# Performance work log

Hardware: AMD Instinct MI355X
Metric: run time of the kernel (lower is better)

## Reference

```python
import jax, jax.numpy as jnp
import numpy as np

B, C, H, W = 8, 512, 48, 48
DK = C // 8            # query/key dim
L = max(H, W)          # rel_pos_length == H == W
R = 2 * L - 1          # num relative shifts
N = H * W
EPS = 1e-5


def setup_inputs() -> dict:
    key = jax.random.key(0)
    ks = jax.random.split(key, 20)
    d = {
        "x": jax.random.normal(ks[0], (B, C, H, W), jnp.float32),
        "Wq": jax.random.normal(ks[1], (DK, C), jnp.float32) * 0.02,
        "bq": jnp.zeros((DK,), jnp.float32),
        "q_scale": jnp.ones((DK,), jnp.float32),
        "q_bias": jnp.zeros((DK,), jnp.float32),
        "Wk": jax.random.normal(ks[2], (DK, C), jnp.float32) * 0.02,
        "bk": jnp.zeros((DK,), jnp.float32),
        "k_scale": jnp.ones((DK,), jnp.float32),
        "k_bias": jnp.zeros((DK,), jnp.float32),
        "Wv": jax.random.normal(ks[3], (C, C), jnp.float32) * 0.02,
        "bv": jnp.zeros((C,), jnp.float32),
        "v_scale": jnp.ones((C,), jnp.float32),
        "v_bias": jnp.zeros((C,), jnp.float32),
        "rel_rows": jax.random.normal(ks[4], (R, DK), jnp.float32),
        "rel_columns": jax.random.normal(ks[5], (R, DK), jnp.float32),
        "bnr_scale": jnp.ones((C,), jnp.float32),
        "bnr_bias": jnp.zeros((C,), jnp.float32),
        "bnc_scale": jnp.ones((C,), jnp.float32),
        "bnc_bias": jnp.zeros((C,), jnp.float32),
        # gamma is a learned scalar (init 0 in torch; nonzero here so output != x)
        "gamma": jax.random.normal(ks[6], (1,), jnp.float32) * 0.1,
    }
    return d


def _bn(y, scale, bias):
    # train-mode BatchNorm2d: batch stats over (B,H,W), biased variance
    m = jnp.mean(y, axis=(0, 2, 3))
    v = jnp.mean((y - m[None, :, None, None]) ** 2, axis=(0, 2, 3))
    yn = (y - m[None, :, None, None]) * jax.lax.rsqrt(v + EPS)[None, :, None, None]
    return yn * scale[None, :, None, None] + bias[None, :, None, None]


def _conv_bn_relu(x, Wc, bc, scale, bias):
    y = jnp.einsum('bchw,oc->bohw', x, Wc) + bc[None, :, None, None]  # 1x1 conv
    return jax.nn.relu(_bn(y, scale, bias))


def _rel_P(l, rel_table):
    # compute_reindexing_tensor reduces to a one-hot over shift (i - x) since
    # |i-x| <= L always holds when L == l; Ih @ rel_table == gather by shift.
    x = jnp.arange(l)[:, None]
    i = jnp.arange(l)[None, :]
    idx = i - x + (L - 1)                 # (l, l) in [0, 2L-2]
    return rel_table[idx]                 # (l, l, DK)


def reference(x, Wq, bq, q_scale, q_bias, Wk, bk, k_scale, k_bias,
              Wv, bv, v_scale, v_bias, rel_rows, rel_columns,
              bnr_scale, bnr_bias, bnc_scale, bnc_bias, gamma):
    q = _conv_bn_relu(x, Wq, bq, q_scale, q_bias).reshape(B, DK, N)   # proj_query^T
    k = _conv_bn_relu(x, Wk, bk, k_scale, k_bias).reshape(B, DK, N)
    v = _conv_bn_relu(x, Wv, bv, v_scale, v_bias).reshape(B, C, N)

    energy = jnp.einsum('bdn,bdm->bnm', q, k)        # (B,N,N) = Q^T K (unscaled)
    attention = jax.nn.softmax(energy, axis=-1)
    out = jnp.einsum('bcj,bij->bci', v, attention)   # V A^T
    attn_mask = out.reshape(B, C, H, W)

    # relative position terms: Eh = V (Ph Q^T), Ew = V (Pw Q^T)
    Ph = _rel_P(H, rel_rows).reshape(N, DK)          # (N,DK) since H==W
    Mh = jnp.einsum('nd,bdm->bnm', Ph, q)
    Eh = jnp.einsum('bcn,bnm->bcm', v, Mh).reshape(B, C, H, W)
    Eh = _bn(Eh, bnr_scale, bnr_bias)

    Pw = _rel_P(W, rel_columns).reshape(N, DK)
    Mw = jnp.einsum('nd,bdm->bnm', Pw, q)
    Ew = jnp.einsum('bcn,bnm->bcm', v, Mw).reshape(B, C, H, W)
    Ew = _bn(Ew, bnc_scale, bnc_bias)

    attn_mask = attn_mask + Eh + Ew
    return gamma[0] * attn_mask + x
```

## Files before the change

kernel.cpp:

```cpp
#include <hip/hip_runtime.h>
#include <math.h>

#define BB   8
#define CIN  512
#define NSP  2304
#define OCH  640
#define LL   48

#define AS1 __attribute__((address_space(1)))
#define AS3 __attribute__((address_space(3)))

typedef __attribute__((ext_vector_type(8))) short bf16x8;
typedef __attribute__((ext_vector_type(8))) unsigned short u16x8;
typedef __attribute__((ext_vector_type(4))) float f32x4;

__device__ inline unsigned short f2bf(float f) {
  unsigned int u = __float_as_uint(f);
  unsigned int r = (u + 0x7fffu + ((u >> 16) & 1u)) >> 16;
  return (unsigned short)r;
}
__device__ inline float bf2f(unsigned short h) {
  return __uint_as_float(((unsigned int)h) << 16);
}


#define STAGE128x64(GP, LD, LDSN)                                              \
  {                                                                            \
    const unsigned short* gsrc_ = (GP);                                        \
    _Pragma("unroll") for (int cc_ = 0; cc_ < 4; cc_++) {                      \
      int base_ = w * 2048 + cc_ * 512;                                        \
      int row_ = w * 32 + cc_ * 8 + rsub;                                      \
      __builtin_amdgcn_global_load_lds(                                        \
          (const AS1 void*)(gsrc_ + (size_t)row_ * (LD) + scolb),              \
          (AS3 void*)&(LDSN)[base_], 16, 0, 0);                                \
    }                                                                          \
  }

#define STAGE8(GPA, LDA, LA, GPB, LDB, LB)                                     \
  {                                                                            \
    if (w < 4) {                                                               \
      const unsigned short* gsrc_ = (GPA);                                     \
      _Pragma("unroll") for (int cc_ = 0; cc_ < 4; cc_++) {                    \
        int base_ = w * 2048 + cc_ * 512;                                      \
        int row_ = w * 32 + cc_ * 8 + rsub;                                    \
        __builtin_amdgcn_global_load_lds(                                      \
            (const AS1 void*)(gsrc_ + (size_t)row_ * (LDA) + scolb),           \
            (AS3 void*)&(LA)[base_], 16, 0, 0);                                \
      }                                                                        \
    } else {                                                                   \
      const unsigned short* gsrc_ = (GPB);                                     \
      int w2_ = w - 4;                                                         \
      _Pragma("unroll") for (int cc_ = 0; cc_ < 4; cc_++) {                    \
        int base_ = w2_ * 2048 + cc_ * 512;                                    \
        int row_ = w2_ * 32 + cc_ * 8 + rsub;                                  \
        __builtin_amdgcn_global_load_lds(                                      \
            (const AS1 void*)(gsrc_ + (size_t)row_ * (LDB) + scolb),           \
            (AS3 void*)&(LB)[base_], 16, 0, 0);                                \
      }                                                                        \
    }                                                                          \
  }

#define MFMA_STEP(APTR, BPTR)                                                  \
  _Pragma("unroll") for (int kk_ = 0; kk_ < 2; kk_++) {                        \
    bf16x8 af_[4], bf_[4];                                                     \
    int kcol_ = (((kk_ * 4 + (lane >> 4)) ^ (lane & 7)) * 8);                  \
    _Pragma("unroll") for (int m_ = 0; m_ < 4; m_++)                           \
      af_[m_] = *(const bf16x8*)&(APTR)[(wr * 64 + m_ * 16 + (lane & 15)) * 64 + kcol_]; \
    _Pragma("unroll") for (int n_ = 0; n_ < 4; n_++)                           \
      bf_[n_] = *(const bf16x8*)&(BPTR)[(wc * 64 + n_ * 16 + (lane & 15)) * 64 + kcol_]; \
    _Pragma("unroll") for (int m_ = 0; m_ < 4; m_++)                           \
      _Pragma("unroll") for (int n_ = 0; n_ < 4; n_++)                         \
        acc[m_][n_] = __builtin_amdgcn_mfma_f32_16x16x32_bf16(                 \
            af_[m_], bf_[n_], acc[m_][n_], 0, 0, 0);                           \
  }

#define MFMA_STEP8(APTR, BPTR)                                                 \
  _Pragma("unroll") for (int kk_ = 0; kk_ < 2; kk_++) {                        \
    bf16x8 af_[4], bf_[2];                                                     \
    int kcol_ = (((kk_ * 4 + (lane >> 4)) ^ (lane & 7)) * 8);                  \
    _Pragma("unroll") for (int m_ = 0; m_ < 4; m_++)                           \
      af_[m_] = *(const bf16x8*)&(APTR)[(wr * 64 + m_ * 16 + (lane & 15)) * 64 + kcol_]; \
    _Pragma("unroll") for (int n_ = 0; n_ < 2; n_++)                           \
      bf_[n_] = *(const bf16x8*)&(BPTR)[(wc * 32 + n_ * 16 + (lane & 15)) * 64 + kcol_]; \
    _Pragma("unroll") for (int m_ = 0; m_ < 4; m_++)                           \
      _Pragma("unroll") for (int n_ = 0; n_ < 2; n_++)                         \
        acc[m_][n_] = __builtin_amdgcn_mfma_f32_16x16x32_bf16(                 \
            af_[m_], bf_[n_], acc[m_][n_], 0, 0, 0);                           \
  }

#define MFMA_PROLOG()                                                          \
  const int tid = threadIdx.x;                                                 \
  const int lane = tid & 63;                                                   \
  const int w = tid >> 6;                                                      \
  const int wr = w >> 1, wc = w & 1;                                           \
  const int rsub = lane >> 3;                                                  \
  const int scolb = ((lane & 7) ^ rsub) * 8;                                   \
  f32x4 acc[4][4] = {};                                                        \
  (void)scolb; (void)rsub; (void)wr; (void)wc;

__global__ __launch_bounds__(256) void prep_all(
    const float* __restrict__ Wq, const float* __restrict__ bq,
    const float* __restrict__ Wk, const float* __restrict__ bk,
    const float* __restrict__ Wv, const float* __restrict__ bv,
    const float* __restrict__ rel_rows, const float* __restrict__ rel_cols,
    unsigned short* __restrict__ Wstb, float* __restrict__ bst,
    unsigned short* __restrict__ Pcatb) {
  int idx = blockIdx.x * 256 + threadIdx.x;
  if (idx < OCH * CIN) {
    int row = idx >> 9;
    float val;
    if (row < 64)       val = Wq[idx];
    else if (row < 128) val = Wk[idx - (64 << 9)];
    else                val = Wv[idx - (128 << 9)];
    Wstb[idx] = f2bf(val);
    if (idx < OCH) {
      float bval;
      if (idx < 64)       bval = bq[idx];
      else if (idx < 128) bval = bk[idx - 64];
      else                bval = bv[idx - 128];
      bst[idx] = bval;
    }
  } else {
    int p = idx - OCH * CIN;
    int dd = p / NSP;
    int n = p - dd * NSP;
    int xr = n / LL;
    int ic = n - xr * LL;
    int shift = ic - xr + (LL - 1);
    float val = (dd < 64) ? rel_rows[shift * 64 + dd]
                          : rel_cols[shift * 64 + (dd - 64)];
    Pcatb[p] = f2bf(val);
  }
}

__global__ __launch_bounds__(256) void transpose_x(
    const float* __restrict__ x, unsigned short* __restrict__ xTb) {
  __shared__ float t[64][65];
  const int n0 = blockIdx.x * 64;
  const int c0 = blockIdx.y * 64;
  const int b = blockIdx.z;
  const int j = threadIdx.x & 63;
  const int g = threadIdx.x >> 6;
  const float* xp = x + (size_t)b * CIN * NSP;
#pragma unroll
  for (int i = 0; i < 16; i++) {
    int cl = g * 16 + i;
    t[cl][j] = xp[(size_t)(c0 + cl) * NSP + n0 + j];
  }
  __syncthreads();
  unsigned short* op = xTb + (size_t)b * NSP * CIN;
#pragma unroll
  for (int i = 0; i < 16; i++) {
    int nl = g * 16 + i;
    op[(size_t)(n0 + nl) * CIN + c0 + j] = f2bf(t[j][nl]);
  }
}

__global__ __launch_bounds__(256) void proj_mfma(
    const unsigned short* __restrict__ Wstb, const float* __restrict__ bst,
    const unsigned short* __restrict__ xTb, unsigned short* __restrict__ y16,
    float* __restrict__ part1, float* __restrict__ part2) {
  __shared__ unsigned short As[2][8192];
  __shared__ unsigned short Bs[2][8192];
  int sw = ((blockIdx.x & 7) * 90) + (blockIdx.x >> 3);
  const int rb = sw % 5;
  const int nb = (sw / 5) % 18;
  const int b = sw / 90;
  const int r0 = rb * 128;
// ... 116 lines not shown
    ushort4 o0, o1;
    o0.x = f2bf(fmaxf(0.f, a * bf2f(u0.x) + bo));
    o0.y = f2bf(fmaxf(0.f, a * bf2f(u0.y) + bo));
    o0.z = f2bf(fmaxf(0.f, a * bf2f(u0.z) + bo));
    o0.w = f2bf(fmaxf(0.f, a * bf2f(u0.w) + bo));
    o1.x = f2bf(fmaxf(0.f, a * bf2f(u1.x) + bo));
    o1.y = f2bf(fmaxf(0.f, a * bf2f(u1.y) + bo));
    o1.z = f2bf(fmaxf(0.f, a * bf2f(u1.z) + bo));
    o1.w = f2bf(fmaxf(0.f, a * bf2f(u1.w) + bo));
    *(ushort4*)&y16[off] = o0;
    *(ushort4*)&y16[off + 4] = o1;
    if (ch < 128) {
      *(ushort4*)&qk[ch][n8] = o0;
      *(ushort4*)&qk[ch][n8 + 4] = o1;
    }
  }
  __syncthreads();
#pragma unroll
  for (int it = 0; it < 4; it++) {
    int combo = (tid >> 6) + it * 4;
    int plane = combo >> 3;
    int dg = combo & 7;
    int nl = tid & 63;
    unsigned short tmp[8];
#pragma unroll
    for (int d = 0; d < 8; d++) tmp[d] = qk[plane * 64 + dg * 8 + d][nl];
    unsigned short* out = (plane == 0) ? qTb : kTb;
    *(u16x8*)&out[((size_t)b * NSP + n0 + nl) * 64 + dg * 8] = *(u16x8*)tmp;
  }
}

__global__ __launch_bounds__(256) void gq_mfma(
    const unsigned short* __restrict__ y16, float* __restrict__ Gqp,
    float* __restrict__ qsp) {
  __shared__ float wlds[4 * 4096];
  const int bx = blockIdx.x;
  const int b = bx >> 2, kc = bx & 3;
  const int tid = threadIdx.x;
  const int lane = tid & 63;
  const int w = tid >> 6;
  const unsigned short* q = y16 + (size_t)b * OCH * NSP;
  f32x4 acc[4][4] = {};
  for (int k0 = kc * 576 + w * 32; k0 < (kc + 1) * 576; k0 += 128) {
    bf16x8 fr[4];
#pragma unroll
    for (int f = 0; f < 4; f++) {
      int row = f * 16 + (lane & 15);
      fr[f] = *(const bf16x8*)&q[(size_t)row * NSP + k0 + (lane >> 4) * 8];
    }
#pragma unroll
    for (int fm = 0; fm < 4; fm++)
#pragma unroll
      for (int fn = 0; fn < 4; fn++)
        acc[fm][fn] = __builtin_amdgcn_mfma_f32_16x16x32_bf16(
            fr[fm], fr[fn], acc[fm][fn], 0, 0, 0);
  }
#pragma unroll
  for (int fm = 0; fm < 4; fm++)
#pragma unroll
    for (int fn = 0; fn < 4; fn++)
#pragma unroll
      for (int r = 0; r < 4; r++) {
        int d = fm * 16 + (lane >> 4) * 4 + r;
        int e = fn * 16 + (lane & 15);
        wlds[w * 4096 + d * 64 + e] = acc[fm][fn][r];
      }
  {
    float s = 0.f;
    const unsigned short* qrow = q + (size_t)(tid >> 2) * NSP + kc * 576 + (tid & 3) * 144;
    for (int i = 0; i < 144; i += 4) {
      ushort4 u = *(const ushort4*)&qrow[i];
      s += bf2f(u.x) + bf2f(u.y) + bf2f(u.z) + bf2f(u.w);
    }
    s += __shfl_down(s, 1);
    s += __shfl_down(s, 2);
    if ((tid & 3) == 0) qsp[bx * 64 + (tid >> 2)] = s;
  }
  __syncthreads();
  for (int t = tid; t < 4096; t += 256)
    Gqp[(size_t)bx * 4096 + t] =
        wlds[t] + wlds[4096 + t] + wlds[8192 + t] + wlds[12288 + t];
}

__global__ __launch_bounds__(256) void energy_mfma(
    const unsigned short* __restrict__ qTb, const unsigned short* __restrict__ kTb,
    unsigned short* __restrict__ Pp, float* __restrict__ Ppart) {
  __shared__ unsigned short lds[16384];
  __shared__ float rs[256];
  int sw = ((blockIdx.x & 7) * 324) + (blockIdx.x >> 3);
  const int jb = sw % 18;
  const int ib = (sw / 18) % 18;
  const int b = sw / 324;
  const int i0 = ib * 128;
  const int j0 = jb * 128;
  MFMA_PROLOG();
  STAGE128x64(qTb + ((size_t)b * NSP + i0) * 64, 64, lds);
  STAGE128x64(kTb + ((size_t)b * NSP + j0) * 64, 64, (lds + 8192));
  __syncthreads();
  MFMA_STEP(lds, (lds + 8192));
  __syncthreads();
#pragma unroll
  for (int m = 0; m < 4; m++) {
#pragma unroll
    for (int r = 0; r < 4; r++) {
      int rl = wr * 64 + m * 16 + (lane >> 4) * 4 + r;
      float s1 = 0.f;
#pragma unroll
      for (int n = 0; n < 4; n++) {
        unsigned short h = f2bf(__expf(acc[m][n][r]));
        lds[rl * 128 + wc * 64 + n * 16 + (lane & 15)] = h;
        s1 += bf2f(h);
      }
#pragma unroll
      for (int off = 1; off < 16; off <<= 1) s1 += __shfl_xor(s1, off);
      if ((lane & 15) == 0) rs[rl * 2 + wc] = s1;
    }
  }
  __syncthreads();
  unsigned short* pp = Pp + (size_t)b * NSP * NSP;
#pragma unroll
  for (int c8 = tid; c8 < 2048; c8 += 256) {
    int il = c8 >> 4;
    int jl = (c8 & 15) * 8;
    u16x8 v = *(const u16x8*)&lds[il * 128 + jl];
    *(u16x8*)&pp[(size_t)(i0 + il) * NSP + j0 + jl] = v;
  }
  if (tid < 128)
    Ppart[((size_t)b * 18 + jb) * NSP + i0 + tid] = rs[tid * 2] + rs[tid * 2 + 1];
}

__global__ __launch_bounds__(256) void up_mfma(
    const unsigned short* __restrict__ y16, const unsigned short* __restrict__ Pcatb,
    float* __restrict__ Upart) {
  __shared__ unsigned short As[2][8192];
  __shared__ unsigned short Bs[2][8192];
  int sw = ((blockIdx.x & 7) * 24) + (blockIdx.x >> 3);
  const int cb = sw % 4;
  const int kc = (sw / 4) % 6;
  const int b = sw / 24;
  const int c0 = cb * 128;
  MFMA_PROLOG();
  const unsigned short* A = y16 + ((size_t)b * OCH + 128 + c0) * NSP + kc * 384;
  const unsigned short* B = Pcatb + kc * 384;

  STAGE128x64(A, NSP, As[0]);
  STAGE128x64(B, NSP, Bs[0]);
  asm volatile("s_waitcnt vmcnt(0)" ::: "memory");
  __builtin_amdgcn_sched_barrier(0);
  __builtin_amdgcn_s_barrier();

  int cur = 0;
  for (int t = 0; t < 6; ++t) {
    if (t + 1 < 6) {
      STAGE128x64(A + (t + 1) * 64, NSP, As[cur ^ 1]);
      STAGE128x64(B + (t + 1) * 64, NSP, Bs[cur ^ 1]);
    }
    __builtin_amdgcn_s_setprio(1);
    MFMA_STEP(As[cur], Bs[cur]);
    __builtin_amdgcn_s_setprio(0);
    asm volatile("s_waitcnt vmcnt(0)" ::: "memory");
    __builtin_amdgcn_sched_barrier(0);
    __builtin_amdgcn_s_barrier();
    cur ^= 1;
  }

  float* up = Upart + ((size_t)kc * BB + b) * CIN * 128 + (size_t)c0 * 128;
#pragma unroll
  for (int m = 0; m < 4; m++)
#pragma unroll
    for (int r = 0; r < 4; r++) {
      int rl = wr * 64 + m * 16 + (lane >> 4) * 4 + r;
#pragma unroll
      for (int n = 0; n < 4; n++) {
        int col = wc * 64 + n * 16 + (lane & 15);
        up[(size_t)rl * 128 + col] = acc[m][n][r];
      }
    }
}

__global__ __launch_bounds__(256) void rel_finalize(
    const float* __restrict__ Upart, const float* __restrict__ Gqp,
    const float* __restrict__ qsp,
    const float* __restrict__ bnr_s, const float* __restrict__ bnr_b,
    const float* __restrict__ bnc_s, const float* __restrict__ bnc_b,
    float* __restrict__ offc, unsigned short* __restrict__ Ucb) {
  const int c = blockIdx.x;
  const int tid = threadIdx.x;
  __shared__ float U[8][128];
  __shared__ float ghw[2];
  for (int t = tid; t < 1024; t += 256) {
    int b = t >> 7, dd = t & 127;
    float s = 0.f;
#pragma unroll
    for (int kc = 0; kc < 6; kc++)
      s += Upart[(((size_t)kc * BB + b) * CIN + c) * 128 + dd];
    U[b][dd] = s;
  }
  __syncthreads();
  if (tid < 64) {
    const int d = tid;
    float s1h = 0.f, s2h = 0.f, s1w = 0.f, s2w = 0.f;
    for (int b = 0; b < BB; b++) {
      float uh = U[b][d], uw = U[b][64 + d];
      float th = 0.f, tw = 0.f;
      float qsd = 0.f;
#pragma unroll
      for (int kc = 0; kc < 4; kc++) {
        const float* G = Gqp + ((size_t)(b * 4 + kc)) * 4096 + d * 64;
        for (int e = 0; e < 64; e++) {
          float g = G[e];
          th += g * U[b][e];
          tw += g * U[b][64 + e];
        }
        qsd += qsp[(b * 4 + kc) * 64 + d];
      }
      s1h += uh * qsd;
      s2h += uh * th;
      s1w += uw * qsd;
      s2w += uw * tw;
    }
#pragma unroll
    for (int off = 32; off > 0; off >>= 1) {
      s1h += __shfl_down(s1h, off);
      s2h += __shfl_down(s2h, off);
      s1w += __shfl_down(s1w, off);
      s2w += __shfl_down(s2w, off);
    }
    if (d == 0) {
      const float inv = 1.f / (float)(BB * NSP);
      float mh = s1h * inv, vh = s2h * inv - mh * mh;
      float mw = s1w * inv, vw = s2w * inv - mw * mw;
      float gch = bnr_s[c] * rsqrtf(vh + 1e-5f);
      float gcw = bnc_s[c] * rsqrtf(vw + 1e-5f);
      ghw[0] = gch;
      ghw[1] = gcw;
      offc[c] = (bnr_b[c] - mh * gch) + (bnc_b[c] - mw * gcw);
    }
  }
  __syncthreads();
  for (int t = tid; t < 512; t += 256) {
    int b = t >> 6, d = t & 63;
    Ucb[((size_t)b * CIN + c) * 64 + d] =
        f2bf(U[b][d] * ghw[0] + U[b][64 + d] * ghw[1]);
  }
}

__global__ __launch_bounds__(512) void attn_fused_gemm(
    const unsigned short* __restrict__ y16,
    const unsigned short* __restrict__ Pp,
    const float* __restrict__ Ppart,
    const unsigned short* __restrict__ Ucb,
    const unsigned short* __restrict__ qTb,
    const float* __restrict__ offc,
    const float* __restrict__ gammap,
    const float* __restrict__ x,
    float* __restrict__ dst) {
  __shared__ unsigned short As[4][8192];
  __shared__ unsigned short Bs[4][8192];
  __shared__ float rzl[128];
  int sw = ((blockIdx.x & 7) * 72) + (blockIdx.x >> 3);
  const int cb = sw % 4;
  const int ib = (sw / 4) % 18;
  const int b = sw / 72;
  const int c0 = cb * 128;
  const int i0 = ib * 128;
  const int tid = threadIdx.x;
  const int lane = tid & 63;
  const int w = tid >> 6;
  const int wr = w >> 2, wc = w & 3;
  const int rsub = lane >> 3;
  const int scolb = ((lane & 7) ^ rsub) * 8;
  const int l15 = lane & 15, l4 = lane >> 4;
  f32x4 acc[4][2] = {};

  const unsigned short* A = y16 + ((size_t)b * OCH + 128 + c0) * NSP;
  const unsigned short* B = Pp + (size_t)b * NSP * NSP + (size_t)i0 * NSP;
  const unsigned short* A2 = Ucb + (size_t)b * CIN * 64 + (size_t)c0 * 64;
  const unsigned short* B2 = qTb + ((size_t)b * NSP + i0) * 64;

  if (tid < 128) {
    float s = 0.f;
#pragma unroll
    for (int jb = 0; jb < 18; jb++)
      s += Ppart[((size_t)b * 18 + jb) * NSP + i0 + tid];
    rzl[tid] = 1.f / s;
  }
  asm volatile("s_waitcnt lgkmcnt(0)" ::: "memory");
  __builtin_amdgcn_sched_barrier(0);

  STAGE8(A, NSP, As[0], B, NSP, Bs[0]);
  STAGE8(A + 64, NSP, As[1], B + 64, NSP, Bs[1]);

  for (int t = 0; t < 37; ++t) {
    if (t + 2 < 36) {
      STAGE8(A + (t + 2) * 64, NSP, As[(t + 2) & 3], B + (t + 2) * 64, NSP, Bs[(t + 2) & 3]);
      asm volatile("s_waitcnt vmcnt(8)" ::: "memory");
    } else if (t + 2 == 36) {
      STAGE8(A2, 64, As[(t + 2) & 3], B2, 64, Bs[(t + 2) & 3]);
      asm volatile("s_waitcnt vmcnt(8)" ::: "memory");
    } else if (t + 1 <= 36) {
      asm volatile("s_waitcnt vmcnt(4)" ::: "memory");
    } else {
      asm volatile("s_waitcnt vmcnt(0)" ::: "memory");
    }
    __builtin_amdgcn_sched_barrier(0);
    __builtin_amdgcn_s_barrier();
    if (t == 36) {
#pragma unroll
      for (int n = 0; n < 2; n++) {
        float rz = rzl[wc * 32 + n * 16 + l15];
#pragma unroll
        for (int m = 0; m < 4; m++)
#pragma unroll
          for (int r = 0; r < 4; r++) acc[m][n][r] *= rz;
      }
    }
    __builtin_amdgcn_s_setprio(1);
    MFMA_STEP8(As[t & 3], Bs[t & 3]);
    __builtin_amdgcn_s_setprio(0);
  }

  const float gmm = gammap[0];
  const float* xp = x + (size_t)b * CIN * NSP;
  float* dp = dst + (size_t)b * CIN * NSP;
#pragma unroll
  for (int m = 0; m < 4; m++) {
#pragma unroll
    for (int r = 0; r < 4; r++) {
      int c = c0 + wr * 64 + m * 16 + l4 * 4 + r;
      float off = offc[c];
#pragma unroll
      for (int n = 0; n < 2; n++) {
        int i = i0 + wc * 32 + n * 16 + l15;
        size_t o = (size_t)c * NSP + i;
        dp[o] = gmm * (acc[m][n][r] + off) + xp[o];
      }
    }
  }
}

extern "C" void kernel_launch(void* const* d_in, const int* in_sizes, int n_in,
                              void* d_out, int out_size, void* d_ws, size_t ws_size,
                              hipStream_t stream) {
  const float* x        = (const float*)d_in[0];
  const float* Wq       = (const float*)d_in[1];
  const float* bq       = (const float*)d_in[2];
  const float* q_scale  = (const float*)d_in[3];
  const float* q_bias   = (const float*)d_in[4];
  const float* Wk       = (const float*)d_in[5];
  const float* bk       = (const float*)d_in[6];
  const float* k_scale  = (const float*)d_in[7];
  const float* k_bias   = (const float*)d_in[8];
  const float* Wv       = (const float*)d_in[9];
  const float* bv       = (const float*)d_in[10];
  const float* v_scale  = (const float*)d_in[11];
  const float* v_bias   = (const float*)d_in[12];
  const float* rel_rows = (const float*)d_in[13];
  const float* rel_cols = (const float*)d_in[14];
  const float* bnr_s    = (const float*)d_in[15];
  const float* bnr_b    = (const float*)d_in[16];
  const float* bnc_s    = (const float*)d_in[17];
  const float* bnc_b    = (const float*)d_in[18];
  const float* gamma    = (const float*)d_in[19];
  float* dst = (float*)d_out;

  float* ws = (float*)d_ws;
  size_t o = 0;
  unsigned short* Wstb = (unsigned short*)(ws + o); o += (size_t)OCH * CIN / 2;
  float* bst    = ws + o; o += 1024;
  float* chanA  = ws + o; o += 1024;
  float* chanB  = ws + o; o += 1024;
  unsigned short* Pcatb = (unsigned short*)(ws + o); o += (size_t)128 * NSP / 2;
  unsigned short* y16 = (unsigned short*)(ws + o); o += (size_t)BB * OCH * NSP / 2;
  unsigned short* xTb = (unsigned short*)(ws + o); o += (size_t)BB * NSP * CIN / 2;
  unsigned short* Pp  = (unsigned short*)(ws + o); o += (size_t)BB * NSP * NSP / 2;
  float* Ppart  = ws + o; o += (size_t)BB * 18 * NSP;
  float* Upart  = ws + o; o += (size_t)6 * BB * CIN * 128;
  float* Gqp    = ws + o; o += (size_t)32 * 4096;
  float* part1  = ws + o; o += (size_t)BB * 18 * OCH;
  float* part2  = ws + o; o += (size_t)BB * 18 * OCH;
  float* qsp    = ws + o; o += (size_t)32 * 64;
  float* offc   = ws + o; o += 1024;
  unsigned short* qTb = (unsigned short*)(ws + o); o += (size_t)BB * NSP * 64 / 2;
  unsigned short* kTb = (unsigned short*)(ws + o); o += (size_t)BB * NSP * 64 / 2;
  unsigned short* Ucb = (unsigned short*)(ws + o); o += (size_t)BB * CIN * 64 / 2;

  prep_all<<<(OCH * CIN + 128 * NSP) / 256, 256, 0, stream>>>(
      Wq, bq, Wk, bk, Wv, bv, rel_rows, rel_cols, Wstb, bst, Pcatb);
  transpose_x<<<dim3(NSP / 64, CIN / 64, BB), 256, 0, stream>>>(x, xTb);

  proj_mfma<<<720, 256, 0, stream>>>(Wstb, bst, xTb, y16, part1, part2);
  bn_finalize<<<OCH, 256, 0, stream>>>(part1, part2, q_scale, q_bias, k_scale,
                                       k_bias, v_scale, v_bias, chanA, chanB);
  bn_post<<<dim3(36, BB), 256, 0, stream>>>(y16, chanA, chanB, qTb, kTb);
  gq_mfma<<<32, 256, 0, stream>>>(y16, Gqp, qsp);

  energy_mfma<<<2592, 256, 0, stream>>>(qTb, kTb, Pp, Ppart);

  up_mfma<<<192, 256, 0, stream>>>(y16, Pcatb, Upart);
  rel_finalize<<<CIN, 256, 0, stream>>>(Upart, Gqp, qsp, bnr_s, bnr_b,
                                        bnc_s, bnc_b, offc, Ucb);

  attn_fused_gemm<<<576, 512, 0, stream>>>(y16, Pp, Ppart, Ucb, qTb, offc,
                                           gamma, x, dst);
}
```

Baseline: 245.0 us.

## Fuse energy/softmax computation into attention GEMM flash-style, drop materialized P

Removes the separate energy kernel that wrote the full B×N×N bf16 exp(QK^T) matrix plus row partial sums to global memory. The attention kernel now recomputes each 128×64 energy tile from q/k staged in LDS, exponentiates it into an LDS P tile, and accumulates row sums in registers for the final normalization. This avoids roughly 85 MB of global writes and reads. In exchange, exp and QK^T are recomputed once per channel block (4x redundancy), and there are extra barriers per step with only single-buffered V/P.

```diff
diff --git a/kernel.cpp b/kernel.cpp
--- a/kernel.cpp
+++ b/kernel.cpp
@@ -33,30 +33,6 @@
       __builtin_amdgcn_global_load_lds(                                        \
           (const AS1 void*)(gsrc_ + (size_t)row_ * (LD) + scolb),              \
           (AS3 void*)&(LDSN)[base_], 16, 0, 0);                                \
-    }                                                                          \
-  }
-
-#define STAGE8(GPA, LDA, LA, GPB, LDB, LB)                                     \
-  {                                                                            \
-    if (w < 4) {                                                               \
-      const unsigned short* gsrc_ = (GPA);                                     \
-      _Pragma("unroll") for (int cc_ = 0; cc_ < 4; cc_++) {                    \
-        int base_ = w * 2048 + cc_ * 512;                                      \
-        int row_ = w * 32 + cc_ * 8 + rsub;                                    \
-        __builtin_amdgcn_global_load_lds(                                      \
-            (const AS1 void*)(gsrc_ + (size_t)row_ * (LDA) + scolb),           \
-            (AS3 void*)&(LA)[base_], 16, 0, 0);                                \
-      }                                                                        \
-    } else {                                                                   \
-      const unsigned short* gsrc_ = (GPB);                                     \
-      int w2_ = w - 4;                                                         \
-      _Pragma("unroll") for (int cc_ = 0; cc_ < 4; cc_++) {                    \
-        int base_ = w2_ * 2048 + cc_ * 512;                                    \
-        int row_ = w2_ * 32 + cc_ * 8 + rsub;                                  \
-        __builtin_amdgcn_global_load_lds(                                      \
-            (const AS1 void*)(gsrc_ + (size_t)row_ * (LDB) + scolb),           \
-            (AS3 void*)&(LB)[base_], 16, 0, 0);                                \
-      }                                                                        \
     }                                                                          \
   }
 
@@ -366,53 +342,6 @@
         wlds[t] + wlds[4096 + t] + wlds[8192 + t] + wlds[12288 + t];
 }
 
-__global__ __launch_bounds__(256) void energy_mfma(
-    const unsigned short* __restrict__ qTb, const unsigned short* __restrict__ kTb,
-    unsigned short* __restrict__ Pp, float* __restrict__ Ppart) {
-  __shared__ unsigned short lds[16384];
-  __shared__ float rs[256];
-  int sw = ((blockIdx.x & 7) * 324) + (blockIdx.x >> 3);
-  const int jb = sw % 18;
-  const int ib = (sw / 18) % 18;
-  const int b = sw / 324;
-  const int i0 = ib * 128;
-  const int j0 = jb * 128;
-  MFMA_PROLOG();
-  STAGE128x64(qTb + ((size_t)b * NSP + i0) * 64, 64, lds);
-  STAGE128x64(kTb + ((size_t)b * NSP + j0) * 64, 64, (lds + 8192));
-  __syncthreads();
-  MFMA_STEP(lds, (lds + 8192));
-  __syncthreads();
-#pragma unroll
-  for (int m = 0; m < 4; m++) {
-#pragma unroll
-    for (int r = 0; r < 4; r++) {
-      int rl = wr * 64 + m * 16 + (lane >> 4) * 4 + r;
-      float s1 = 0.f;
-#pragma unroll
-      for (int n = 0; n < 4; n++) {
-        unsigned short h = f2bf(__expf(acc[m][n][r]));
-        lds[rl * 128 + wc * 64 + n * 16 + (lane & 15)] = h;
-        s1 += bf2f(h);
-      }
-#pragma unroll
-      for (int off = 1; off < 16; off <<= 1) s1 += __shfl_xor(s1, off);
-      if ((lane & 15) == 0) rs[rl * 2 + wc] = s1;
-    }
-  }
-  __syncthreads();
-  unsigned short* pp = Pp + (size_t)b * NSP * NSP;
-#pragma unroll
-  for (int c8 = tid; c8 < 2048; c8 += 256) {
-    int il = c8 >> 4;
-    int jl = (c8 & 15) * 8;
-    u16x8 v = *(const u16x8*)&lds[il * 128 + jl];
-    *(u16x8*)&pp[(size_t)(i0 + il) * NSP + j0 + jl] = v;
-  }
-  if (tid < 128)
-    Ppart[((size_t)b * 18 + jb) * NSP + i0 + tid] = rs[tid * 2] + rs[tid * 2 + 1];
-}
-
 __global__ __launch_bounds__(256) void up_mfma(
     const unsigned short* __restrict__ y16, const unsigned short* __restrict__ Pcatb,
     float* __restrict__ Upart) {
@@ -529,18 +458,20 @@
   }
 }
 
-__global__ __launch_bounds__(512) void attn_fused_gemm(
+__global__ __launch_bounds__(512) void attn_flash2(
     const unsigned short* __restrict__ y16,
-    const unsigned short* __restrict__ Pp,
-    const float* __restrict__ Ppart,
+    const unsigned short* __restrict__ qTb,
+    const unsigned short* __restrict__ kTb,
     const unsigned short* __restrict__ Ucb,
-    const unsigned short* __restrict__ qTb,
     const float* __restrict__ offc,
     const float* __restrict__ gammap,
     const float* __restrict__ x,
     float* __restrict__ dst) {
-  __shared__ unsigned short As[4][8192];
-  __shared__ unsigned short Bs[4][8192];
+  __shared__ unsigned short q_lds[8192];
+  __shared__ unsigned short k_lds[2][4096];
+  __shared__ unsigned short v_lds[8192];
+  __shared__ unsigned short p_lds[8192];
+  __shared__ float rsum_lds[8][64];
   __shared__ float rzl[128];
   int sw = ((blockIdx.x & 7) * 72) + (blockIdx.x >> 3);
   const int cb = sw % 4;
@@ -552,57 +483,136 @@
   const int lane = tid & 63;
   const int w = tid >> 6;
   const int wr = w >> 2, wc = w & 3;
+  const int iSub = w >> 2, jSub = w & 3;
   const int rsub = lane >> 3;
   const int scolb = ((lane & 7) ^ rsub) * 8;
   const int l15 = lane & 15, l4 = lane >> 4;
   f32x4 acc[4][2] = {};
-
-  const unsigned short* A = y16 + ((size_t)b * OCH + 128 + c0) * NSP;
-  const unsigned short* B = Pp + (size_t)b * NSP * NSP + (size_t)i0 * NSP;
-  const unsigned short* A2 = Ucb + (size_t)b * CIN * 64 + (size_t)c0 * 64;
-  const unsigned short* B2 = qTb + ((size_t)b * NSP + i0) * 64;
-
-  if (tid < 128) {
-    float s = 0.f;
-#pragma unroll
-    for (int jb = 0; jb < 18; jb++)
-      s += Ppart[((size_t)b * 18 + jb) * NSP + i0 + tid];
-    rzl[tid] = 1.f / s;
-  }
-  asm volatile("s_waitcnt lgkmcnt(0)" ::: "memory");
+  float rs[4][4] = {{0.f}};
+
+  const unsigned short* qsrc = qTb + ((size_t)b * NSP + i0) * 64;
+  const unsigned short* ksrc = kTb + (size_t)b * NSP * 64;
+  const unsigned short* vsrc = y16 + ((size_t)b * OCH + 128 + c0) * NSP;
+
+#pragma unroll
+  for (int i = 0; i < 2; i++) {
+    int row = w * 16 + i * 8 + rsub;
+    __builtin_amdgcn_global_load_lds(
+        (const AS1 void*)(qsrc + (size_t)row * 64 + scolb),
+        (AS3 void*)&q_lds[w * 1024 + i * 512], 16, 0, 0);
+  }
+  if (w >= 4) {
+    int w4 = w - 4;
+#pragma unroll
+    for (int i = 0; i < 2; i++) {
+      int row = w4 * 16 + i * 8 + rsub;
+      __builtin_amdgcn_global_load_lds(
+          (const AS1 void*)(ksrc + (size_t)row * 64 + scolb),
+          (AS3 void*)&k_lds[0][w4 * 1024 + i * 512], 16, 0, 0);
+    }
+  }
+  asm volatile("s_waitcnt vmcnt(0)" ::: "memory");
   __builtin_amdgcn_sched_barrier(0);
-
-  STAGE8(A, NSP, As[0], B, NSP, Bs[0]);
-  STAGE8(A + 64, NSP, As[1], B + 64, NSP, Bs[1]);
-
-  for (int t = 0; t < 37; ++t) {
-    if (t + 2 < 36) {
-      STAGE8(A + (t + 2) * 64, NSP, As[(t + 2) & 3], B + (t + 2) * 64, NSP, Bs[(t + 2) & 3]);
-      asm volatile("s_waitcnt vmcnt(8)" ::: "memory");
-    } else if (t + 2 == 36) {
-      STAGE8(A2, 64, As[(t + 2) & 3], B2, 64, Bs[(t + 2) & 3]);
-      asm volatile("s_waitcnt vmcnt(8)" ::: "memory");
-    } else if (t + 1 <= 36) {
-      asm volatile("s_waitcnt vmcnt(4)" ::: "memory");
-    } else {
-      asm volatile("s_waitcnt vmcnt(0)" ::: "memory");
-    }
+  __builtin_amdgcn_s_barrier();
+
+  for (int t = 0; t < 36; ++t) {
+    const int cur = t & 1;
+    if (w < 4) {
+#pragma unroll
+      for (int cc = 0; cc < 4; cc++) {
+        int row = w * 32 + cc * 8 + rsub;
+        __builtin_amdgcn_global_load_lds(
+            (const AS1 void*)(vsrc + (size_t)row * NSP + t * 64 + scolb),
+            (AS3 void*)&v_lds[w * 2048 + cc * 512], 16, 0, 0);
+      }
+    } else if (t + 1 < 36) {
+      int w4 = w - 4;
+#pragma unroll
+      for (int i = 0; i < 2; i++) {
+        int row = (t + 1) * 64 + w4 * 16 + i * 8 + rsub;
+        __builtin_amdgcn_global_load_lds(
+            (const AS1 void*)(ksrc + (size_t)row * 64 + scolb),
+            (AS3 void*)&k_lds[cur ^ 1][w4 * 1024 + i * 512], 16, 0, 0);
+      }
+    }
+    f32x4 eacc[4] = {};
+#pragma unroll
+    for (int kk = 0; kk < 2; kk++) {
+      int kcol = ((kk * 4 + l4) ^ (lane & 7)) * 8;
+      bf16x8 bk = *(const bf16x8*)&k_lds[cur][(jSub * 16 + l15) * 64 + kcol];
+#pragma unroll
+      for (int m = 0; m < 4; m++) {
+        bf16x8 aq = *(const bf16x8*)&q_lds[(iSub * 64 + m * 16 + l15) * 64 + kcol];
+        eacc[m] = __builtin_amdgcn_mfma_f32_16x16x32_bf16(aq, bk, eacc[m], 0, 0, 0);
+      }
+    }
+#pragma unroll
+    for (int m = 0; m < 4; m++) {
+#pragma unroll
+      for (int r = 0; r < 4; r++) {
+        float p = __expf(eacc[m][r]);
+        unsigned short h = f2bf(p);
+        rs[m][r] += bf2f(h);
+        int il = iSub * 64 + m * 16 + l4 * 4 + r;
+        int j = jSub * 16 + l15;
+        p_lds[il * 64 + ((j >> 3) ^ (il & 7)) * 8 + (j & 7)] = h;
+      }
+    }
+    asm volatile("s_waitcnt lgkmcnt(0)" ::: "memory");
+    if (w < 4) asm volatile("s_waitcnt vmcnt(0)" ::: "memory");
     __builtin_amdgcn_sched_barrier(0);
     __builtin_amdgcn_s_barrier();
-    if (t == 36) {
-#pragma unroll
-      for (int n = 0; n < 2; n++) {
-        float rz = rzl[wc * 32 + n * 16 + l15];
-#pragma unroll
-        for (int m = 0; m < 4; m++)
-#pragma unroll
-          for (int r = 0; r < 4; r++) acc[m][n][r] *= rz;
-      }
-    }
     __builtin_amdgcn_s_setprio(1);
-    MFMA_STEP8(As[t & 3], Bs[t & 3]);
+    MFMA_STEP8(v_lds, p_lds);
     __builtin_amdgcn_s_setprio(0);
-  }
+    if (w >= 4) asm volatile("s_waitcnt vmcnt(0)" ::: "memory");
+    __builtin_amdgcn_sched_barrier(0);
+    __builtin_amdgcn_s_barrier();
+  }
+
+  if (w < 4) {
+    const unsigned short* a2 = Ucb + (size_t)b * CIN * 64 + (size_t)c0 * 64;
+#pragma unroll
+    for (int cc = 0; cc < 4; cc++) {
+      int row = w * 32 + cc * 8 + rsub;
+      __builtin_amdgcn_global_load_lds(
+          (const AS1 void*)(a2 + (size_t)row * 64 + scolb),
+          (AS3 void*)&v_lds[w * 2048 + cc * 512], 16, 0, 0);
+    }
+  }
+#pragma unroll
+  for (int m = 0; m < 4; m++) {
+#pragma unroll
+    for (int r = 0; r < 4; r++) {
+      float s = rs[m][r];
+      s += __shfl_xor(s, 1);
+      s += __shfl_xor(s, 2);
+      s += __shfl_xor(s, 4);
+      s += __shfl_xor(s, 8);
+      if (l15 == 0) rsum_lds[w][m * 16 + l4 * 4 + r] = s;
+    }
+  }
+  asm volatile("s_waitcnt lgkmcnt(0)" ::: "memory");
+  if (w < 4) asm volatile("s_waitcnt vmcnt(0)" ::: "memory");
+  __builtin_amdgcn_sched_barrier(0);
+  __builtin_amdgcn_s_barrier();
+  if (tid < 128) {
+    int is = tid >> 6, il = tid & 63;
+    rzl[tid] = 1.f / (rsum_lds[is * 4 + 0][il] + rsum_lds[is * 4 + 1][il] +
+                      rsum_lds[is * 4 + 2][il] + rsum_lds[is * 4 + 3][il]);
+  }
+  __syncthreads();
+
+#pragma unroll
+  for (int n = 0; n < 2; n++) {
+    float rz = rzl[wc * 32 + n * 16 + l15];
+#pragma unroll
+    for (int m = 0; m < 4; m++)
+#pragma unroll
+      for (int r = 0; r < 4; r++) acc[m][n][r] *= rz;
+  }
+
+  MFMA_STEP8(v_lds, q_lds);
 
   const float gmm = gammap[0];
   const float* xp = x + (size_t)b * CIN * NSP;
@@ -657,8 +667,6 @@
   unsigned short* Pcatb = (unsigned short*)(ws + o); o += (size_t)128 * NSP / 2;
   unsigned short* y16 = (unsigned short*)(ws + o); o += (size_t)BB * OCH * NSP / 2;
   unsigned short* xTb = (unsigned short*)(ws + o); o += (size_t)BB * NSP * CIN / 2;
-  unsigned short* Pp  = (unsigned short*)(ws + o); o += (size_t)BB * NSP * NSP / 2;
-  float* Ppart  = ws + o; o += (size_t)BB * 18 * NSP;
   float* Upart  = ws + o; o += (size_t)6 * BB * CIN * 128;
   float* Gqp    = ws + o; o += (size_t)32 * 4096;
   float* part1  = ws + o; o += (size_t)BB * 18 * OCH;
@@ -679,12 +687,9 @@
   bn_post<<<dim3(36, BB), 256, 0, stream>>>(y16, chanA, chanB, qTb, kTb);
   gq_mfma<<<32, 256, 0, stream>>>(y16, Gqp, qsp);
 
-  energy_mfma<<<2592, 256, 0, stream>>>(qTb, kTb, Pp, Ppart);
-
   up_mfma<<<192, 256, 0, stream>>>(y16, Pcatb, Upart);
   rel_finalize<<<CIN, 256, 0, stream>>>(Upart, Gqp, qsp, bnr_s, bnr_b,
                                         bnc_s, bnc_b, offc, Ucb);
 
-  attn_fused_gemm<<<576, 512, 0, stream>>>(y16, Pp, Ppart, Ucb, qTb, offc,
-                                           gamma, x, dst);
-}
+  attn_flash2<<<576, 512, 0, stream>>>(y16, qTb, kTb, Ucb, offc, gamma, x, dst);
+}
```

Measured after the change: 302.4 us. 23.4% more time.

## Widen attn_fused_gemm tile to 128x256 with double-buffered LDS pipeline

Applied to the files above, without the earlier changes.

The final fused attention GEMM now computes a 128-channel by 256-position output tile per block instead of 128x128. This halves the grid to 288 blocks and doubles the per-wave accumulator tile to 4x4 MFMA fragments. The 4-stage, prefetch-distance-2 LDS ring is replaced by a simple double buffer that waits on all loads after each step. The larger tile is meant to cut repeated reads of the A operand (y16 V rows) and raise MFMA work per LDS load. The trade-off is higher register pressure, fewer blocks than CUs for occupancy, and a shallower prefetch that may expose memory latency.

```diff
diff --git a/kernel.cpp b/kernel.cpp
--- a/kernel.cpp
+++ b/kernel.cpp
@@ -36,30 +36,6 @@
     }                                                                          \
   }
 
-#define STAGE8(GPA, LDA, LA, GPB, LDB, LB)                                     \
-  {                                                                            \
-    if (w < 4) {                                                               \
-      const unsigned short* gsrc_ = (GPA);                                     \
-      _Pragma("unroll") for (int cc_ = 0; cc_ < 4; cc_++) {                    \
-        int base_ = w * 2048 + cc_ * 512;                                      \
-        int row_ = w * 32 + cc_ * 8 + rsub;                                    \
-        __builtin_amdgcn_global_load_lds(                                      \
-            (const AS1 void*)(gsrc_ + (size_t)row_ * (LDA) + scolb),           \
-            (AS3 void*)&(LA)[base_], 16, 0, 0);                                \
-      }                                                                        \
-    } else {                                                                   \
-      const unsigned short* gsrc_ = (GPB);                                     \
-      int w2_ = w - 4;                                                         \
-      _Pragma("unroll") for (int cc_ = 0; cc_ < 4; cc_++) {                    \
-        int base_ = w2_ * 2048 + cc_ * 512;                                    \
-        int row_ = w2_ * 32 + cc_ * 8 + rsub;                                  \
-        __builtin_amdgcn_global_load_lds(                                      \
-            (const AS1 void*)(gsrc_ + (size_t)row_ * (LDB) + scolb),           \
-            (AS3 void*)&(LB)[base_], 16, 0, 0);                                \
-      }                                                                        \
-    }                                                                          \
-  }
-
 #define MFMA_STEP(APTR, BPTR)                                                  \
   _Pragma("unroll") for (int kk_ = 0; kk_ < 2; kk_++) {                        \
     bf16x8 af_[4], bf_[4];                                                     \
@@ -70,20 +46,6 @@
       bf_[n_] = *(const bf16x8*)&(BPTR)[(wc * 64 + n_ * 16 + (lane & 15)) * 64 + kcol_]; \
     _Pragma("unroll") for (int m_ = 0; m_ < 4; m_++)                           \
       _Pragma("unroll") for (int n_ = 0; n_ < 4; n_++)                         \
-        acc[m_][n_] = __builtin_amdgcn_mfma_f32_16x16x32_bf16(                 \
-            af_[m_], bf_[n_], acc[m_][n_], 0, 0, 0);                           \
-  }
-
-#define MFMA_STEP8(APTR, BPTR)                                                 \
-  _Pragma("unroll") for (int kk_ = 0; kk_ < 2; kk_++) {                        \
-    bf16x8 af_[4], bf_[2];                                                     \
-    int kcol_ = (((kk_ * 4 + (lane >> 4)) ^ (lane & 7)) * 8);                  \
-    _Pragma("unroll") for (int m_ = 0; m_ < 4; m_++)                           \
-      af_[m_] = *(const bf16x8*)&(APTR)[(wr * 64 + m_ * 16 + (lane & 15)) * 64 + kcol_]; \
-    _Pragma("unroll") for (int n_ = 0; n_ < 2; n_++)                           \
-      bf_[n_] = *(const bf16x8*)&(BPTR)[(wc * 32 + n_ * 16 + (lane & 15)) * 64 + kcol_]; \
-    _Pragma("unroll") for (int m_ = 0; m_ < 4; m_++)                           \
-      _Pragma("unroll") for (int n_ = 0; n_ < 2; n_++)                         \
         acc[m_][n_] = __builtin_amdgcn_mfma_f32_16x16x32_bf16(                 \
             af_[m_], bf_[n_], acc[m_][n_], 0, 0, 0);                           \
   }
@@ -539,15 +501,15 @@
     const float* __restrict__ gammap,
     const float* __restrict__ x,
     float* __restrict__ dst) {
-  __shared__ unsigned short As[4][8192];
-  __shared__ unsigned short Bs[4][8192];
-  __shared__ float rzl[128];
-  int sw = ((blockIdx.x & 7) * 72) + (blockIdx.x >> 3);
+  __shared__ unsigned short As[2][8192];
+  __shared__ unsigned short Bs[2][16384];
+  __shared__ float rzl[256];
+  int sw = ((blockIdx.x & 7) * 36) + (blockIdx.x >> 3);
   const int cb = sw % 4;
-  const int ib = (sw / 4) % 18;
-  const int b = sw / 72;
+  const int ib = (sw / 4) % 9;
+  const int b = sw / 36;
   const int c0 = cb * 128;
-  const int i0 = ib * 128;
+  const int i0 = ib * 256;
   const int tid = threadIdx.x;
   const int lane = tid & 63;
   const int w = tid >> 6;
@@ -555,53 +517,71 @@
   const int rsub = lane >> 3;
   const int scolb = ((lane & 7) ^ rsub) * 8;
   const int l15 = lane & 15, l4 = lane >> 4;
-  f32x4 acc[4][2] = {};
+  f32x4 acc[4][4] = {};
 
   const unsigned short* A = y16 + ((size_t)b * OCH + 128 + c0) * NSP;
   const unsigned short* B = Pp + (size_t)b * NSP * NSP + (size_t)i0 * NSP;
   const unsigned short* A2 = Ucb + (size_t)b * CIN * 64 + (size_t)c0 * 64;
   const unsigned short* B2 = qTb + ((size_t)b * NSP + i0) * 64;
 
-  if (tid < 128) {
+#define STAGEF(GPA, LDA, LA, GPB, LDB, LB)                                     \
+  {                                                                            \
+    if (w < 4) {                                                               \
+      const unsigned short* ga_ = (GPA);                                       \
+      _Pragma("unroll") for (int cc_ = 0; cc_ < 4; cc_++) {                    \
+        int row_ = w * 32 + cc_ * 8 + rsub;                                    \
+        __builtin_amdgcn_global_load_lds(                                      \
+            (const AS1 void*)(ga_ + (size_t)row_ * (LDA) + scolb),             \
+            (AS3 void*)&(LA)[w * 2048 + cc_ * 512], 16, 0, 0);                 \
+      }                                                                        \
+    }                                                                          \
+    {                                                                          \
+      const unsigned short* gb_ = (GPB);                                       \
+      _Pragma("unroll") for (int cc_ = 0; cc_ < 4; cc_++) {                    \
+        int row_ = w * 32 + cc_ * 8 + rsub;                                    \
+        __builtin_amdgcn_global_load_lds(                                      \
+            (const AS1 void*)(gb_ + (size_t)row_ * (LDB) + scolb),             \
+            (AS3 void*)&(LB)[w * 2048 + cc_ * 512], 16, 0, 0);                 \
+      }                                                                        \
+    }                                                                          \
+  }
+
+  if (tid < 256) {
     float s = 0.f;
 #pragma unroll
     for (int jb = 0; jb < 18; jb++)
       s += Ppart[((size_t)b * 18 + jb) * NSP + i0 + tid];
     rzl[tid] = 1.f / s;
   }
-  asm volatile("s_waitcnt lgkmcnt(0)" ::: "memory");
+  STAGEF(A, NSP, As[0], B, NSP, Bs[0]);
+  asm volatile("s_waitcnt vmcnt(0)" ::: "memory");
   __builtin_amdgcn_sched_barrier(0);
-
-  STAGE8(A, NSP, As[0], B, NSP, Bs[0]);
-  STAGE8(A + 64, NSP, As[1], B + 64, NSP, Bs[1]);
-
+  __builtin_amdgcn_s_barrier();
+
+  int cur = 0;
   for (int t = 0; t < 37; ++t) {
-    if (t + 2 < 36) {
-      STAGE8(A + (t + 2) * 64, NSP, As[(t + 2) & 3], B + (t + 2) * 64, NSP, Bs[(t + 2) & 3]);
-      asm volatile("s_waitcnt vmcnt(8)" ::: "memory");
-    } else if (t + 2 == 36) {
-      STAGE8(A2, 64, As[(t + 2) & 3], B2, 64, Bs[(t + 2) & 3]);
-      asm volatile("s_waitcnt vmcnt(8)" ::: "memory");
-    } else if (t + 1 <= 36) {
-      asm volatile("s_waitcnt vmcnt(4)" ::: "memory");
-    } else {
-      asm volatile("s_waitcnt vmcnt(0)" ::: "memory");
-    }
+    if (t + 1 < 36) {
+      STAGEF(A + (t + 1) * 64, NSP, As[cur ^ 1], B + (t + 1) * 64, NSP, Bs[cur ^ 1]);
+    } else if (t + 1 == 36) {
+      STAGEF(A2, 64, As[cur ^ 1], B2, 64, Bs[cur ^ 1]);
+    }
+    if (t == 36) {
+#pragma unroll
+      for (int n = 0; n < 4; n++) {
+        float rz = rzl[wc * 64 + n * 16 + l15];
+#pragma unroll
+        for (int m = 0; m < 4; m++)
+#pragma unroll
+          for (int r = 0; r < 4; r++) acc[m][n][r] *= rz;
+      }
+    }
+    __builtin_amdgcn_s_setprio(1);
+    MFMA_STEP(As[cur], Bs[cur]);
+    __builtin_amdgcn_s_setprio(0);
+    asm volatile("s_waitcnt vmcnt(0)" ::: "memory");
     __builtin_amdgcn_sched_barrier(0);
     __builtin_amdgcn_s_barrier();
-    if (t == 36) {
-#pragma unroll
-      for (int n = 0; n < 2; n++) {
-        float rz = rzl[wc * 32 + n * 16 + l15];
-#pragma unroll
-        for (int m = 0; m < 4; m++)
-#pragma unroll
-          for (int r = 0; r < 4; r++) acc[m][n][r] *= rz;
-      }
-    }
-    __builtin_amdgcn_s_setprio(1);
-    MFMA_STEP8(As[t & 3], Bs[t & 3]);
-    __builtin_amdgcn_s_setprio(0);
+    cur ^= 1;
   }
 
   const float gmm = gammap[0];
@@ -614,13 +594,14 @@
       int c = c0 + wr * 64 + m * 16 + l4 * 4 + r;
       float off = offc[c];
 #pragma unroll
-      for (int n = 0; n < 2; n++) {
-        int i = i0 + wc * 32 + n * 16 + l15;
+      for (int n = 0; n < 4; n++) {
+        int i = i0 + wc * 64 + n * 16 + l15;
         size_t o = (size_t)c * NSP + i;
         dp[o] = gmm * (acc[m][n][r] + off) + xp[o];
       }
     }
   }
+#undef STAGEF
 }
 
 extern "C" void kernel_launch(void* const* d_in, const int* in_sizes, int n_in,
@@ -685,6 +666,6 @@
   rel_finalize<<<CIN, 256, 0, stream>>>(Upart, Gqp, qsp, bnr_s, bnr_b,
                                         bnc_s, bnc_b, offc, Ucb);
 
-  attn_fused_gemm<<<576, 512, 0, stream>>>(y16, Pp, Ppart, Ucb, qTb, offc,
+  attn_fused_gemm<<<288, 512, 0, stream>>>(y16, Pp, Ppart, Ucb, qTb, offc,
                                            gamma, x, dst);
 }
```

After: 267.0 us. 9.0% more time.

## Widen energy tiles to 128x256 with 512 threads; double-buffer fused attention GEMM

Applied to the files above, without the earlier changes.

The energy kernel now computes a 128x256 tile per 512-thread block, so each Q tile is loaded once and reused across two K tiles. Loads go directly to LDS, and the exp/bf16 write-out is done in two halves that reuse the K buffer. The fused attention GEMM drops from a 4-stage pipeline with a 2-ahead prefetch to a 2-stage double buffer that waits on vmcnt(0) every iteration. This halves that kernel's LDS use, which may raise occupancy, but it hides less memory latency.

```diff
diff --git a/kernel.cpp b/kernel.cpp
--- a/kernel.cpp
+++ b/kernel.cpp
@@ -366,51 +366,110 @@
         wlds[t] + wlds[4096 + t] + wlds[8192 + t] + wlds[12288 + t];
 }
 
-__global__ __launch_bounds__(256) void energy_mfma(
+__global__ __launch_bounds__(512) void energy_mfma(
     const unsigned short* __restrict__ qTb, const unsigned short* __restrict__ kTb,
     unsigned short* __restrict__ Pp, float* __restrict__ Ppart) {
-  __shared__ unsigned short lds[16384];
-  __shared__ float rs[256];
-  int sw = ((blockIdx.x & 7) * 324) + (blockIdx.x >> 3);
-  const int jb = sw % 18;
-  const int ib = (sw / 18) % 18;
-  const int b = sw / 324;
+  __shared__ unsigned short q_lds[8192];
+  __shared__ unsigned short k_lds[16384];
+  __shared__ float rs_lds[4][128];
+  int sw = ((blockIdx.x & 7) * 162) + (blockIdx.x >> 3);
+  const int jp = sw % 9;
+  const int ib = (sw / 9) % 18;
+  const int b = sw / 162;
   const int i0 = ib * 128;
-  const int j0 = jb * 128;
-  MFMA_PROLOG();
-  STAGE128x64(qTb + ((size_t)b * NSP + i0) * 64, 64, lds);
-  STAGE128x64(kTb + ((size_t)b * NSP + j0) * 64, 64, (lds + 8192));
-  __syncthreads();
-  MFMA_STEP(lds, (lds + 8192));
-  __syncthreads();
-#pragma unroll
-  for (int m = 0; m < 4; m++) {
-#pragma unroll
-    for (int r = 0; r < 4; r++) {
-      int rl = wr * 64 + m * 16 + (lane >> 4) * 4 + r;
-      float s1 = 0.f;
-#pragma unroll
-      for (int n = 0; n < 4; n++) {
-        unsigned short h = f2bf(__expf(acc[m][n][r]));
-        lds[rl * 128 + wc * 64 + n * 16 + (lane & 15)] = h;
-        s1 += bf2f(h);
-      }
-#pragma unroll
-      for (int off = 1; off < 16; off <<= 1) s1 += __shfl_xor(s1, off);
-      if ((lane & 15) == 0) rs[rl * 2 + wc] = s1;
-    }
-  }
-  __syncthreads();
+  const int j0 = jp * 256;
+  const int tid = threadIdx.x;
+  const int lane = tid & 63;
+  const int w = tid >> 6;
+  const int wr = w >> 2, wc = w & 3;
+  const int rsub = lane >> 3;
+  const int scolb = ((lane & 7) ^ rsub) * 8;
+  const int l15 = lane & 15, l4 = lane >> 4;
+  f32x4 acc[4][4] = {};
+
+  if (w < 4) {
+    const unsigned short* gq = qTb + ((size_t)b * NSP + i0) * 64;
+#pragma unroll
+    for (int cc = 0; cc < 4; cc++) {
+      int row = w * 32 + cc * 8 + rsub;
+      __builtin_amdgcn_global_load_lds(
+          (const AS1 void*)(gq + (size_t)row * 64 + scolb),
+          (AS3 void*)&q_lds[w * 2048 + cc * 512], 16, 0, 0);
+    }
+  }
+  {
+    const unsigned short* gk = kTb + ((size_t)b * NSP + j0) * 64;
+#pragma unroll
+    for (int cc = 0; cc < 4; cc++) {
+      int row = w * 32 + cc * 8 + rsub;
+      __builtin_amdgcn_global_load_lds(
+          (const AS1 void*)(gk + (size_t)row * 64 + scolb),
+          (AS3 void*)&k_lds[w * 2048 + cc * 512], 16, 0, 0);
+    }
+  }
+  asm volatile("s_waitcnt vmcnt(0)" ::: "memory");
+  __builtin_amdgcn_sched_barrier(0);
+  __builtin_amdgcn_s_barrier();
+
+#pragma unroll
+  for (int kk = 0; kk < 2; kk++) {
+    bf16x8 af[4], bf[4];
+    int kcol = ((kk * 4 + l4) ^ (lane & 7)) * 8;
+#pragma unroll
+    for (int m = 0; m < 4; m++)
+      af[m] = *(const bf16x8*)&q_lds[(wr * 64 + m * 16 + l15) * 64 + kcol];
+#pragma unroll
+    for (int n = 0; n < 4; n++)
+      bf[n] = *(const bf16x8*)&k_lds[(wc * 64 + n * 16 + l15) * 64 + kcol];
+#pragma unroll
+    for (int m = 0; m < 4; m++)
+#pragma unroll
+      for (int n = 0; n < 4; n++)
+        acc[m][n] = __builtin_amdgcn_mfma_f32_16x16x32_bf16(
+            af[m], bf[n], acc[m][n], 0, 0, 0);
+  }
+  __builtin_amdgcn_s_barrier();
+
   unsigned short* pp = Pp + (size_t)b * NSP * NSP;
 #pragma unroll
-  for (int c8 = tid; c8 < 2048; c8 += 256) {
-    int il = c8 >> 4;
-    int jl = (c8 & 15) * 8;
-    u16x8 v = *(const u16x8*)&lds[il * 128 + jl];
-    *(u16x8*)&pp[(size_t)(i0 + il) * NSP + j0 + jl] = v;
-  }
-  if (tid < 128)
-    Ppart[((size_t)b * 18 + jb) * NSP + i0 + tid] = rs[tid * 2] + rs[tid * 2 + 1];
+  for (int h = 0; h < 2; h++) {
+    if ((wc >> 1) == h) {
+#pragma unroll
+      for (int m = 0; m < 4; m++) {
+#pragma unroll
+        for (int r = 0; r < 4; r++) {
+          int rl = wr * 64 + m * 16 + l4 * 4 + r;
+          float s1 = 0.f;
+#pragma unroll
+          for (int n = 0; n < 4; n++) {
+            unsigned short hh = f2bf(__expf(acc[m][n][r]));
+            k_lds[rl * 128 + (wc & 1) * 64 + n * 16 + l15] = hh;
+            s1 += bf2f(hh);
+          }
+#pragma unroll
+          for (int off = 1; off < 16; off <<= 1) s1 += __shfl_xor(s1, off);
+          if (l15 == 0) rs_lds[wc][rl] = s1;
+        }
+      }
+    }
+    asm volatile("s_waitcnt lgkmcnt(0)" ::: "memory");
+    __builtin_amdgcn_sched_barrier(0);
+    __builtin_amdgcn_s_barrier();
+#pragma unroll
+    for (int it = 0; it < 4; it++) {
+      int c8 = tid + it * 512;
+      int il = c8 >> 4;
+      int jl = (c8 & 15) * 8;
+      u16x8 v = *(const u16x8*)&k_lds[il * 128 + jl];
+      *(u16x8*)&pp[(size_t)(i0 + il) * NSP + j0 + h * 128 + jl] = v;
+    }
+    __builtin_amdgcn_s_barrier();
+  }
+  if (tid < 256) {
+    int jbh = tid >> 7, i = tid & 127;
+    Ppart[((size_t)b * 18 + jp * 2 + jbh) * NSP + i0 + i] =
+        rs_lds[jbh * 2][i] + rs_lds[jbh * 2 + 1][i];
+  }
 }
 
 __global__ __launch_bounds__(256) void up_mfma(
@@ -539,8 +598,8 @@
     const float* __restrict__ gammap,
     const float* __restrict__ x,
     float* __restrict__ dst) {
-  __shared__ unsigned short As[4][8192];
-  __shared__ unsigned short Bs[4][8192];
+  __shared__ unsigned short As[2][8192];
+  __shared__ unsigned short Bs[2][8192];
   __shared__ float rzl[128];
   int sw = ((blockIdx.x & 7) * 72) + (blockIdx.x >> 3);
   const int cb = sw % 4;
@@ -573,35 +632,34 @@
   __builtin_amdgcn_sched_barrier(0);
 
   STAGE8(A, NSP, As[0], B, NSP, Bs[0]);
-  STAGE8(A + 64, NSP, As[1], B + 64, NSP, Bs[1]);
-
-  for (int t = 0; t < 37; ++t) {
-    if (t + 2 < 36) {
-      STAGE8(A + (t + 2) * 64, NSP, As[(t + 2) & 3], B + (t + 2) * 64, NSP, Bs[(t + 2) & 3]);
-      asm volatile("s_waitcnt vmcnt(8)" ::: "memory");
-    } else if (t + 2 == 36) {
-      STAGE8(A2, 64, As[(t + 2) & 3], B2, 64, Bs[(t + 2) & 3]);
-      asm volatile("s_waitcnt vmcnt(8)" ::: "memory");
-    } else if (t + 1 <= 36) {
-      asm volatile("s_waitcnt vmcnt(4)" ::: "memory");
-    } else {
-      asm volatile("s_waitcnt vmcnt(0)" ::: "memory");
-    }
+  asm volatile("s_waitcnt vmcnt(0)" ::: "memory");
+  __builtin_amdgcn_sched_barrier(0);
+  __builtin_amdgcn_s_barrier();
+
+  int cur = 0;
+  for (int tt = 0; tt < 37; ++tt) {
+    if (tt + 1 < 36) {
+      STAGE8(A + (tt + 1) * 64, NSP, As[cur ^ 1], B + (tt + 1) * 64, NSP, Bs[cur ^ 1]);
+    } else if (tt + 1 == 36) {
+      STAGE8(A2, 64, As[cur ^ 1], B2, 64, Bs[cur ^ 1]);
+    }
+    if (tt == 36) {
+#pragma unroll
+      for (int n = 0; n < 2; n++) {
+        float rz = rzl[wc * 32 + n * 16 + l15];
+#pragma unroll
+        for (int m = 0; m < 4; m++)
+#pragma unroll
+          for (int r = 0; r < 4; r++) acc[m][n][r] *= rz;
+      }
+    }
+    __builtin_amdgcn_s_setprio(1);
+    MFMA_STEP8(As[cur], Bs[cur]);
+    __builtin_amdgcn_s_setprio(0);
+    asm volatile("s_waitcnt vmcnt(0)" ::: "memory");
     __builtin_amdgcn_sched_barrier(0);
     __builtin_amdgcn_s_barrier();
-    if (t == 36) {
-#pragma unroll
-      for (int n = 0; n < 2; n++) {
-        float rz = rzl[wc * 32 + n * 16 + l15];
-#pragma unroll
-        for (int m = 0; m < 4; m++)
-#pragma unroll
-          for (int r = 0; r < 4; r++) acc[m][n][r] *= rz;
-      }
-    }
-    __builtin_amdgcn_s_setprio(1);
-    MFMA_STEP8(As[t & 3], Bs[t & 3]);
-    __builtin_amdgcn_s_setprio(0);
+    cur ^= 1;
   }
 
   const float gmm = gammap[0];
@@ -679,7 +737,7 @@
   bn_post<<<dim3(36, BB), 256, 0, stream>>>(y16, chanA, chanB, qTb, kTb);
   gq_mfma<<<32, 256, 0, stream>>>(y16, Gqp, qsp);
 
-  energy_mfma<<<2592, 256, 0, stream>>>(qTb, kTb, Pp, Ppart);
+  energy_mfma<<<1296, 512, 0, stream>>>(qTb, kTb, Pp, Ppart);
 
   up_mfma<<<192, 256, 0, stream>>>(y16, Pcatb, Upart);
   rel_finalize<<<CIN, 256, 0, stream>>>(Upart, Gqp, qsp, bnr_s, bnr_b,
```

Result: no change. 247.0 us (+0.8%).
